# Optimization experiments

Hardware: AMD Instinct MI355X
Metric: run time of the kernel (lower is better)

## Reference

```python
import jax, jax.numpy as jnp
from jax import lax
import numpy as np

N3, N2, N1, N0 = 862, 1723, 3445, 6890  # mesh hierarchy (SMPL 6890 verts)
DEG, K = 16, 4  # nnz/row per Chebyshev support; K = order 3 + 1 supports


def _conv(x, w, b, s):
    y = lax.conv_general_dilated(x, w, (s, s), 'VALID', dimension_numbers=('NCHW', 'OIHW', 'NCHW'))
    return y + b[None, :, None, None]


def _pool(x):
    return lax.reduce_window(x, -jnp.inf, lax.max, (1, 1, 2, 2), (1, 1, 2, 2), 'VALID')


def _lin(x, w, b):
    return x @ w.T + b


def _rodrigues(r):  # [J,3] axis-angle -> [J,3,3] (batch_rodrigues)
    th = jnp.linalg.norm(r, axis=1, keepdims=True) + 1e-8
    k = r / th
    kx, ky, kz = k[:, 0], k[:, 1], k[:, 2]
    z = jnp.zeros_like(kx)
    Km = jnp.stack([z, -kz, ky, kz, z, -kx, -ky, kx, z], axis=1).reshape(-1, 3, 3)
    th = th[:, :, None]
    return jnp.eye(3, dtype=r.dtype)[None] + jnp.sin(th) * Km + (1.0 - jnp.cos(th)) * (Km @ Km)


def _spmm(idx, val, x):  # torch.sparse.mm with fixed nnz/row; idx,val: [N,D]
    return jnp.einsum('nd,ndf->nf', val, x[idx])


def _gcl(x, idx, val, W, b):  # Chebyshev graph conv: sum_k (A_k @ x) @ W_k + b
    return jnp.einsum('knd,kndf,kfo->no', val, x[idx], W) + b


def _basenet(frame, p):
    (c1w, c1b, c2w, c2b, c3w, c3b, c4w, c4b, c5w, c5b, fc1w, fc1b, fc4w, fc4b) = p
    c = _pool(jax.nn.relu(_conv(frame, c1w, c1b, 2)))
    c = _pool(jax.nn.relu(_conv(c, c2w, c2b, 1)))
    c = _pool(jax.nn.relu(_conv(c, c3w, c3b, 1)))
    c = _pool(jax.nn.relu(_conv(c, c4w, c4b, 1)))
    c = _pool(_conv(c, c5w, c5b, 1))  # [1,128,14,14]
    flat = jnp.transpose(c, (0, 3, 2, 1)).reshape(1, -1)  # torch.transpose(c,1,-1).reshape(1,-1)
    return _lin(flat, fc1w, fc1b), jax.nn.relu(_lin(flat, fc4w, fc4b))


def _forward(segmentations, poses, pose_mean, trans,
             c1w, c1b, c2w, c2b, c3w, c3b, c4w, c4b, c5w, c5b,
             fc1w, fc1b, fc2w, fc2b, fc3w, fc3b, fc4w, fc4b,
             fc5w, fc5b, fc6w, fc6b, fc7w, fc7b,
             gW3, gb3, gW2, gb2, gW1, gb1, gW0, gb0,
             av3, av2, av1, av0, uv2, uv1, uv0,
             ai3, ai2, ai1, ai0, ui2, ui1, ui0):
    nf = segmentations.shape[0]
    bp = (c1w, c1b, c2w, c2b, c3w, c3b, c4w, c4b, c5w, c5b, fc1w, fc1b, fc4w, fc4b)
    shape20, pose200 = jax.vmap(lambda f: _basenet(f, bp))(segmentations)  # [F,1,20],[F,1,200]
    pose_feat = jax.nn.relu(_lin(poses, fc5w, fc5b))  # [F,1,200]
    cat = jnp.concatenate([pose200, pose_feat], axis=-1)  # [F,1,400]
    pose_results = _lin(_lin(cat, fc6w, fc6b), fc7w, fc7b)  # [F,1,219]
    pm = pose_mean.at[:3].set(0.0)
    pose_init = _rodrigues(pm.reshape(-1, 3)).reshape(-1)  # [216]
    pct = jnp.concatenate([trans, pose_init])[None, None]  # [1,1,219]
    add = pose_results + pct
    add_poses = add[..., 3:].reshape(nf, -1, 24, 3, 3)
    add_trans = add[..., :3]
    betas_avr = shape20.reshape(-1, 20).mean(0)  # [20]
    betas_val = _lin(betas_avr, fc3w, fc3b)[None]  # [1,10]
    x = _lin(betas_avr, fc2w, fc2b).reshape(N3, 64)
    x = jax.nn.relu(_gcl(x, ai3, av3, gW3, gb3))  # [862,32]
    x = _spmm(ui2, uv2, x)                         # [1723,32]
    x = jax.nn.relu(_gcl(x, ai2, av2, gW2, gb2))  # [1723,16]
    x = _spmm(ui1, uv1, x)                         # [3445,16]
    x = jax.nn.relu(_gcl(x, ai1, av1, gW1, gb1))  # [3445,16]
    x = _spmm(ui0, uv0, x)                         # [6890,16]
    x = jnp.tanh(_gcl(x, ai0, av0, gW0, gb0))     # [6890,3]
    offsets = (x / 10.0)[None]
    return offsets, betas_val, add_poses, add_trans


def setup_inputs():
    ks = iter(jax.random.split(jax.random.key(0), 80))
    f32 = jnp.float32
    nrm = lambda shp, s: jax.random.normal(next(ks), shp, f32) * s
    uni = lambda shp, s: jax.random.uniform(next(ks), shp, f32) * s
    ri = lambda shp, hi: jax.random.randint(next(ks), shp, 0, hi)
    inp = {}
    inp['segmentations'] = nrm((8, 1, 3, 1017, 1017), 1.0)
    inp['poses'] = nrm((8, 1, 75), 1.0)
    inp['pose_mean'] = nrm((72,), 0.3)
    inp['trans'] = jnp.array([0.0, 0.2, -2.3], f32)
    for nm, shp, s in [('c1w', (8, 3, 3, 3), .1), ('c1b', (8,), .01), ('c2w', (16, 8, 3, 3), .1), ('c2b', (16,), .01),
                       ('c3w', (32, 16, 3, 3), .1), ('c3b', (32,), .01), ('c4w', (64, 32, 3, 3), .1), ('c4b', (64,), .01),
                       ('c5w', (128, 64, 3, 3), .1), ('c5b', (128,), .01),
                       ('fc1w', (20, 25088), .01), ('fc1b', (20,), .01), ('fc2w', (55168, 20), .05), ('fc2b', (55168,), .01),
                       ('fc3w', (10, 20), .05), ('fc3b', (10,), .01), ('fc4w', (200, 25088), .01), ('fc4b', (200,), .01),
                       ('fc5w', (200, 75), .05), ('fc5b', (200,), .01), ('fc6w', (100, 400), .05), ('fc6b', (100,), .01),
                       ('fc7w', (219, 100), .05), ('fc7b', (219,), .01),
                       ('gW3', (4, 64, 32), .1), ('gb3', (32,), .01), ('gW2', (4, 32, 16), .1), ('gb2', (16,), .01),
                       ('gW1', (4, 16, 16), .1), ('gb1', (16,), .01), ('gW0', (4, 16, 3), .1), ('gb0', (3,), .01)]:
        inp[nm] = nrm(shp, s)
    for nm, n in [('3', N3), ('2', N2), ('1', N1), ('0', N0)]:
        inp['av' + nm] = uni((K, n, DEG), 0.2)
        inp['ai' + nm] = ri((K, n, DEG), n)
    for nm, n_fine, n_coarse in [('2', N2, N3), ('1', N1, N2), ('0', N0, N1)]:
        inp['uv' + nm] = uni((n_fine, 4), 0.3)
        inp['ui' + nm] = ri((n_fine, 4), n_coarse)
    return inp


def reference(segmentations, poses, pose_mean, trans,
              c1w, c1b, c2w, c2b, c3w, c3b, c4w, c4b, c5w, c5b,
              fc1w, fc1b, fc2w, fc2b, fc3w, fc3b, fc4w, fc4b,
              fc5w, fc5b, fc6w, fc6b, fc7w, fc7b,
              gW3, gb3, gW2, gb2, gW1, gb1, gW0, gb0,
              av3, av2, av1, av0, uv2, uv1, uv0,
              ai3, ai2, ai1, ai0, ui2, ui1, ui0):
    return _forward(segmentations, poses, pose_mean, trans,
                    c1w, c1b, c2w, c2b, c3w, c3b, c4w, c4b, c5w, c5b,
                    fc1w, fc1b, fc2w, fc2b, fc3w, fc3b, fc4w, fc4b,
                    fc5w, fc5b, fc6w, fc6b, fc7w, fc7b,
                    gW3, gb3, gW2, gb2, gW1, gb1, gW0, gb0,
                    av3, av2, av1, av0, uv2, uv1, uv0,
                    ai3, ai2, ai1, ai0, ui2, ui1, ui0)
```

## Files before the change

### kernel.cpp

```cpp
#include <hip/hip_runtime.h>
#include <math.h>

__global__ __launch_bounds__(256) void conv1_lds(
    const float* __restrict__ in, const float* __restrict__ w,
    const float* __restrict__ bias, float* __restrict__ out)
{
    constexpr int Hin = 1017, P = 254;
    __shared__ float li[17][4][65];
    const int f  = blockIdx.y;
    const int ct = blockIdx.x & 3;
    const int rt = blockIdx.x >> 2;
    const int t  = threadIdx.x;
    const int lane = t & 63, wid = t >> 6;
    const int row0 = rt * 16, col0 = ct * 256;
    const float* inf = in + (size_t)f * 3 * Hin * Hin;

    const int ph = rt * 4 + wid, pw = ct * 64 + lane;
    const bool wactive = (ph < P) && (pw < P);

    float acc[32];
    #pragma unroll
    for (int i = 0; i < 32; i++) acc[i] = 0.f;

    for (int ic = 0; ic < 3; ic++) {
        __syncthreads();
        const float* src = inf + (size_t)ic * Hin * Hin;
        #pragma unroll
        for (int i = 0; i < 17; i++) {
            int gr = row0 + i; if (gr > Hin - 1) gr = Hin - 1;
            int gc = col0 + t; if (gc > Hin - 1) gc = Hin - 1;
            li[i][t & 3][t >> 2] = src[(size_t)gr * Hin + gc];
        }
        if (t < 17) {
            int gr = row0 + t; if (gr > Hin - 1) gr = Hin - 1;
            int gc = col0 + 256; if (gc > Hin - 1) gc = Hin - 1;
            li[t][0][64] = src[(size_t)gr * Hin + gc];
        }
        __syncthreads();

        float win[25];
        #pragma unroll
        for (int r = 0; r < 5; r++)
            #pragma unroll
            for (int c = 0; c < 5; c++)
                win[r * 5 + c] = li[4 * wid + r][c & 3][lane + (c >> 2)];

        #pragma unroll
        for (int oc = 0; oc < 8; oc++) {
            float wr[9];
            #pragma unroll
            for (int j = 0; j < 9; j++) wr[j] = w[(oc * 3 + ic) * 9 + j];
            #pragma unroll
            for (int py = 0; py < 2; py++)
                #pragma unroll
                for (int px = 0; px < 2; px++) {
                    float s = acc[(oc * 2 + py) * 2 + px];
                    #pragma unroll
                    for (int kh = 0; kh < 3; kh++)
                        #pragma unroll
                        for (int kw = 0; kw < 3; kw++)
                            s += wr[kh * 3 + kw] * win[(2 * py + kh) * 5 + (2 * px + kw)];
                    acc[(oc * 2 + py) * 2 + px] = s;
                }
        }
    }

    if (wactive) {
        #pragma unroll
        for (int oc = 0; oc < 8; oc++) {
            float m = fmaxf(fmaxf(acc[oc * 4 + 0], acc[oc * 4 + 1]),
                            fmaxf(acc[oc * 4 + 2], acc[oc * 4 + 3]));
            m = fmaxf(m + bias[oc], 0.f);
            out[(((size_t)f * 8 + oc) * P + ph) * P + pw] = m;
        }
    }
}

template<int IC, int OCG, bool RELU, bool FLATOUT>
__global__ __launch_bounds__(256) void conv_pool_s1(
    const float* __restrict__ in, const float* __restrict__ w,
    const float* __restrict__ bias, float* __restrict__ out,
    int Hin, int P, int OC)
{
    const int f = blockIdx.y, g = blockIdx.z;
    int tid = blockIdx.x * 256 + threadIdx.x;
    if (tid >= P * P) return;
    int ph = tid / P, pw = tid % P;
    const float* inf = in + ((size_t)f * IC) * Hin * Hin + (size_t)(2 * ph) * Hin + 2 * pw;
    const float* wg = w + (size_t)g * OCG * IC * 9;

    float acc[OCG * 4];
    #pragma unroll
    for (int i = 0; i < OCG * 4; i++) acc[i] = 0.f;

    for (int ic = 0; ic < IC; ic++) {
        const float* p = inf + (size_t)ic * Hin * Hin;
        float win[4][4];
        #pragma unroll
        for (int r = 0; r < 4; r++) {
            float2 a = *(const float2*)(p + (size_t)r * Hin);
            float2 b = *(const float2*)(p + (size_t)r * Hin + 2);
            win[r][0] = a.x; win[r][1] = a.y; win[r][2] = b.x; win[r][3] = b.y;
        }
        #pragma unroll
        for (int oc = 0; oc < OCG; oc++) {
            float wr[9];
            #pragma unroll
            for (int j = 0; j < 9; j++) wr[j] = wg[(oc * IC + ic) * 9 + j];
            #pragma unroll
            for (int py = 0; py < 2; py++)
                #pragma unroll
                for (int px = 0; px < 2; px++) {
                    float s = acc[(oc * 2 + py) * 2 + px];
                    #pragma unroll
                    for (int kh = 0; kh < 3; kh++)
                        #pragma unroll
                        for (int kw = 0; kw < 3; kw++)
                            s += wr[kh * 3 + kw] * win[py + kh][px + kw];
                    acc[(oc * 2 + py) * 2 + px] = s;
                }
        }
    }

    #pragma unroll
    for (int oc = 0; oc < OCG; oc++) {
        float m = fmaxf(fmaxf(acc[oc * 4 + 0], acc[oc * 4 + 1]),
                        fmaxf(acc[oc * 4 + 2], acc[oc * 4 + 3]));
        m += bias[g * OCG + oc];
        if (RELU) m = fmaxf(m, 0.f);
        int ocg = g * OCG + oc;
        if (FLATOUT) {
            out[(size_t)f * (P * P * OC) + (pw * P + ph) * OC + ocg] = m;
        } else {
            out[(((size_t)f * OC + ocg) * P + ph) * P + pw] = m;
        }
    }
}

__global__ __launch_bounds__(256) void fc_head_plus(
    const float* __restrict__ flat,
    const float* __restrict__ fc1w, const float* __restrict__ fc1b,
    const float* __restrict__ fc4w, const float* __restrict__ fc4b,
    const float* __restrict__ poses,
    const float* __restrict__ fc5w, const float* __restrict__ fc5b,
    float* __restrict__ shape20, float* __restrict__ pose200,
    float* __restrict__ pose_feat)
{
    int o = blockIdx.x;
    if (o < 220) {
        const float* W = (o < 20) ? fc1w + (size_t)o * 25088
                                  : fc4w + (size_t)(o - 20) * 25088;
        const float4* W4  = (const float4*)W;
        const float4* fl4 = (const float4*)flat;
        float acc[8];
        #pragma unroll
        for (int f = 0; f < 8; f++) acc[f] = 0.f;
        for (int i = threadIdx.x; i < 6272; i += 256) {
            float4 wv = W4[i];
            #pragma unroll
            for (int f = 0; f < 8; f++) {
                float4 xv = fl4[f * 6272 + i];
                acc[f] += wv.x * xv.x + wv.y * xv.y + wv.z * xv.z + wv.w * xv.w;
            }
        }
        #pragma unroll
        for (int f = 0; f < 8; f++)
            for (int off = 32; off > 0; off >>= 1)
                acc[f] += __shfl_down(acc[f], off, 64);
        __shared__ float red[4][8];
        int wid = threadIdx.x >> 6, lane = threadIdx.x & 63;
        if (lane == 0) {
            #pragma unroll
            for (int f = 0; f < 8; f++) red[wid][f] = acc[f];
        }
        __syncthreads();
        if (threadIdx.x < 8) {
            int f = threadIdx.x;
            float s = red[0][f] + red[1][f] + red[2][f] + red[3][f];
            if (o < 20) shape20[f * 20 + o] = s + fc1b[o];
            else        pose200[f * 200 + (o - 20)] = fmaxf(s + fc4b[o - 20], 0.f);
        }
    } else {
        int t = (o - 220) * 256 + threadIdx.x;
        if (t >= 8 * 200) return;
        int f = t / 200, oo = t % 200;
        float s = fc5b[oo];
        const float* pr = poses + f * 75;
        const float* wr = fc5w + oo * 75;
        #pragma unroll 5
        for (int j = 0; j < 75; j++) s += pr[j] * wr[j];
        pose_feat[f * 200 + oo] = fmaxf(s, 0.f);
    }
}

__global__ __launch_bounds__(256) void mid_fused(
    const float* __restrict__ shape20,
    const float* __restrict__ fc2w, const float* __restrict__ fc2b,
    const float* __restrict__ fc3w, const float* __restrict__ fc3b,
    float* __restrict__ x0, float* __restrict__ out,
    const float* __restrict__ pose200, const float* __restrict__ pose_feat,
    const float* __restrict__ fc6w, const float* __restrict__ fc6b,
    float* __restrict__ t1)
{
    int b = blockIdx.x, t = threadIdx.x;
    if (b < 216) {
        __shared__ float avr[20];
        if (t < 20) {
            float s = 0.f;
            for (int f = 0; f < 8; f++) s += shape20[f * 20 + t];
            avr[t] = s * 0.125f;
        }
        __syncthreads();
        int r = b * 256 + t;
        if (r < 55168) {
            float s = fc2b[r];
            const float4* w4 = (const float4*)(fc2w + (size_t)r * 20);
            #pragma unroll
            for (int q = 0; q < 5; q++) {
                float4 wv = w4[q];
                s += wv.x * avr[q * 4 + 0] + wv.y * avr[q * 4 + 1]
                   + wv.z * avr[q * 4 + 2] + wv.w * avr[q * 4 + 3];
            }
            x0[r] = s;
        }
        if (b == 0 && t < 10) {
            float s = fc3b[t];
            for (int j = 0; j < 20; j++) s += fc3w[t * 20 + j] * avr[j];
            out[20670 + t] = s;
        }
    } else {
        int wv = (b - 216) * 4 + (t >> 6);
        int lane = t & 63;
        if (wv >= 8 * 100) return;
        int f = wv / 100, o = wv % 100;
        float s = 0.f;
        for (int j = lane; j < 400; j += 64) {
            float xv = (j < 200) ? pose200[f * 200 + j] : pose_feat[f * 200 + (j - 200)];
            s += xv * fc6w[o * 400 + j];
        }
        #pragma unroll
        for (int off = 32; off > 0; off >>= 1) s += __shfl_down(s, off, 64);
        if (lane == 0) t1[f * 100 + o] = s + fc6b[o];
    }
}

__global__ __launch_bounds__(256) void fc7_gcl3(
    const float* __restrict__ x0, const int* __restrict__ ai3,
    const float* __restrict__ av3, const float* __restrict__ gW3,
    const float* __restrict__ gb3, float* __restrict__ y3,
    const float* __restrict__ t1, const float* __restrict__ fc7w,
    const float* __restrict__ fc7b, const float* __restrict__ pose_mean,
    const float* __restrict__ trans, float* __restrict__ out)
{
    constexpr int F = 64, O = 32, N = 862;
    __shared__ float h[256];
    __shared__ float pp[256];
    const int b = blockIdx.x;
    const int wid = threadIdx.x >> 6, lane = threadIdx.x & 63;

    if (b < N) {
        const int n = b;
        {
            const int k = wid;
            const int*   ip = ai3 + ((size_t)k * N + n) * 16;
            const float* vp = av3 + ((size_t)k * N + n) * 16;
            float s = 0.f;
            #pragma unroll
            for (int d = 0; d < 16; d++)
                s += vp[d] * x0[(size_t)ip[d] * F + lane];
            h[k * F + lane] = s;
        }
        __syncthreads();
        const int t = threadIdx.x;
        const int o = t & 31, part = t >> 5;
        {
            float s = 0.f;
            const int base = part * 32;
            #pragma unroll 8
            for (int i = 0; i < 32; i++)
                s += h[base + i] * gW3[(size_t)(base + i) * O + o];
            pp[t] = s;
        }
        __syncthreads();
        if (t < O) {
            float s = gb3[t];
            #pragma unroll
            for (int p = 0; p < 8; p++) s += pp[p * O + t];
            y3[(size_t)n * O + t] = fmaxf(s, 0.f);
        }
    } else {
        int wv = (b - N) * 4 + wid;
        if (wv >= 8 * 219) return;
        int f = wv / 219, c = wv % 219;
        float s = t1[f * 100 + lane] * fc7w[c * 100 + lane];
        int j2 = lane + 64;
        if (j2 < 100) s += t1[f * 100 + j2] * fc7w[c * 100 + j2];
        #pragma unroll
        for (int off = 32; off > 0; off >>= 1) s += __shfl_down(s, off, 64);
        if (lane != 0) return;
        s += fc7b[c];
        float pct;
        if (c < 3) {
            pct = trans[c];
        } else {
            int j = (c - 3) / 9, e = (c - 3) % 9;
            float rx = (j == 0) ? 0.f : pose_mean[3 * j + 0];
            float ry = (j == 0) ? 0.f : pose_mean[3 * j + 1];
            float rz = (j == 0) ? 0.f : pose_mean[3 * j + 2];
            float th = sqrtf(rx * rx + ry * ry + rz * rz) + 1e-8f;
            float kx = rx / th, ky = ry / th, kz = rz / th;
            float sn = sinf(th), c2 = 1.f - cosf(th);
            float R[9];
            R[0] = 1.f - c2 * (ky * ky + kz * kz);
            R[1] = -sn * kz + c2 * (kx * ky);
            R[2] =  sn * ky + c2 * (kx * kz);
            R[3] =  sn * kz + c2 * (kx * ky);
            R[4] = 1.f - c2 * (kx * kx + kz * kz);
            R[5] = -sn * kx + c2 * (ky * kz);
            R[6] = -sn * ky + c2 * (kx * kz);
            R[7] =  sn * kx + c2 * (ky * kz);
            R[8] = 1.f - c2 * (kx * kx + ky * ky);
            pct = R[e];
        }
        s += pct;
        if (c < 3) out[22408 + f * 3 + c] = s;
        else       out[20680 + f * 216 + (c - 3)] = s;
    }
}

template<int F, int O, int ACT>
__global__ __launch_bounds__(256) void gcl(
    const float* __restrict__ x, const int* __restrict__ ai,
    const float* __restrict__ av, const float* __restrict__ gW,
    const float* __restrict__ gb, float* __restrict__ y, int N)
{
    constexpr int VPB = 64 / F;
    constexpr int OUTS = VPB * O;
    constexpr int PARTS = (256 / OUTS) >= 16 ? 16 :
                          ((256 / OUTS) >= 8 ? 8 :
                          ((256 / OUTS) >= 4 ? 4 : 2));
    constexpr int CH = 4 * F / PARTS;
    constexpr int HS = 4 * F + 4;
    __shared__ float h[VPB][HS];
    __shared__ float pp[OUTS * PARTS];

    const int k = threadIdx.x >> 6;
    const int lane = threadIdx.x & 63;
    const int vl = (VPB == 1) ? 0 : lane / F;
    const int fl = lane % F;
    const int n = blockIdx.x * VPB + vl;
    if (n < N) {
        const int*   ip = ai + ((size_t)k * N + n) * 16;
        const float* vp = av + ((size_t)k * N + n) * 16;
        float s = 0.f;
        #pragma unroll
        for (int d = 0; d < 16; d++)
            s += vp[d] * x[(size_t)ip[d] * F + fl];
        h[vl][k * F + fl] = s;
    }
    __syncthreads();

    const int t = threadIdx.x;
    if (t < OUTS * PARTS) {
        const int idx = t % OUTS;
        const int part = t / OUTS;
        const int v = idx / O, o = idx % O;
        float s = 0.f;
        const int base = part * CH;
        #pragma unroll
        for (int i = 0; i < CH; i++)
            s += h[v][base + i] * gW[(size_t)(base + i) * O + o];
        pp[part * OUTS + idx] = s;
    }
    __syncthreads();
    if (t < OUTS) {
        const int v = t / O, o = t % O;
        const int n2 = blockIdx.x * VPB + v;
        if (n2 < N) {
            float s = gb[o];
            #pragma unroll
            for (int p = 0; p < PARTS; p++) s += pp[p * OUTS + t];
            if (ACT == 0) s = fmaxf(s, 0.f);
            else          s = tanhf(s) * 0.1f;
            y[(size_t)n2 * O + o] = s;
        }
    }
}

template<int F>
__global__ __launch_bounds__(256) void spmm(
    const float* __restrict__ x, const int* __restrict__ ui,
    const float* __restrict__ uv, float* __restrict__ y, int N)
{
    int t = blockIdx.x * 256 + threadIdx.x;
    if (t >= N * F) return;
    int n = t / F, f = t % F;
    float s = 0.f;
    #pragma unroll
    for (int j = 0; j < 4; j++)
        s += uv[n * 4 + j] * x[(size_t)ui[n * 4 + j] * F + f];
    y[t] = s;
}

extern "C" void kernel_launch(void* const* d_in, const int* in_sizes, int n_in,
                              void* d_out, int out_size, void* d_ws, size_t ws_size,
                              hipStream_t stream) {
    (void)in_sizes; (void)n_in; (void)out_size; (void)ws_size;

    const float* seg   = (const float*)d_in[0];
    const float* poses = (const float*)d_in[1];
    const float* pmean = (const float*)d_in[2];
    const float* trans = (const float*)d_in[3];
    const float* c1w = (const float*)d_in[4];  const float* c1b = (const float*)d_in[5];
    const float* c2w = (const float*)d_in[6];  const float* c2b = (const float*)d_in[7];
    const float* c3w = (const float*)d_in[8];  const float* c3b = (const float*)d_in[9];
    const float* c4w = (const float*)d_in[10]; const float* c4b = (const float*)d_in[11];
    const float* c5w = (const float*)d_in[12]; const float* c5b = (const float*)d_in[13];
    const float* fc1w = (const float*)d_in[14]; const float* fc1b = (const float*)d_in[15];
    const float* fc2w = (const float*)d_in[16]; const float* fc2b = (const float*)d_in[17];
    const float* fc3w = (const float*)d_in[18]; const float* fc3b = (const float*)d_in[19];
    const float* fc4w = (const float*)d_in[20]; const float* fc4b = (const float*)d_in[21];
    const float* fc5w = (const float*)d_in[22]; const float* fc5b = (const float*)d_in[23];
    const float* fc6w = (const float*)d_in[24]; const float* fc6b = (const float*)d_in[25];
    const float* fc7w = (const float*)d_in[26]; const float* fc7b = (const float*)d_in[27];
    const float* gW3 = (const float*)d_in[28]; const float* gb3 = (const float*)d_in[29];
    const float* gW2 = (const float*)d_in[30]; const float* gb2 = (const float*)d_in[31];
    const float* gW1 = (const float*)d_in[32]; const float* gb1 = (const float*)d_in[33];
    const float* gW0 = (const float*)d_in[34]; const float* gb0 = (const float*)d_in[35];
    const float* av3 = (const float*)d_in[36]; const int* ai3 = (const int*)d_in[37];
    const float* av2 = (const float*)d_in[38]; const int* ai2 = (const int*)d_in[39];
    const float* av1 = (const float*)d_in[40]; const int* ai1 = (const int*)d_in[41];
    const float* av0 = (const float*)d_in[42]; const int* ai0 = (const int*)d_in[43];
    const float* uv2 = (const float*)d_in[44]; const int* ui2 = (const int*)d_in[45];
    const float* uv1 = (const float*)d_in[46]; const int* ui1 = (const int*)d_in[47];
    const float* uv0 = (const float*)d_in[48]; const int* ui0 = (const int*)d_in[49];

    float* W = (float*)d_ws;
    float* out = (float*)d_out;

    float* pool1 = W + 0;
    float* pool2 = W + 4129024;
    float* pool3 = W + 0;
    float* pool4 = W + 4129024;
    float* flat5 = W + 4589824;
    float* shape20 = W + 1000000;
    float* pose200 = shape20 + 160;
    float* x0  = pose200 + 1600;
    float* y3  = x0 + 55168;
    float* x2  = y3 + 27584;
    float* y2  = x2 + 55136;
    float* x1  = y2 + 27568;
    float* y1  = x1 + 55120;
    float* x0u = y1 + 55120;
    float* pose_feat = x0u + 110240;
    float* t1 = pose_feat + 1600;

    conv1_lds<<<dim3(256, 8), 256, 0, stream>>>(seg, c1w, c1b, pool1);
    conv_pool_s1<8, 8, true, false>
        <<<dim3(63, 8, 2), 256, 0, stream>>>(pool1, c2w, c2b, pool2, 254, 126, 16);
    conv_pool_s1<16, 4, true, false>
        <<<dim3(16, 8, 8), 256, 0, stream>>>(pool2, c3w, c3b, pool3, 126, 62, 32);
    conv_pool_s1<32, 2, true, false>
        <<<dim3(4, 8, 32), 256, 0, stream>>>(pool3, c4w, c4b, pool4, 62, 30, 64);
    conv_pool_s1<64, 2, false, true>
        <<<dim3(1, 8, 64), 256, 0, stream>>>(pool4, c5w, c5b, flat5, 30, 14, 128);

    fc_head_plus<<<dim3(227), 256, 0, stream>>>(flat5, fc1w, fc1b, fc4w, fc4b,
                                                poses, fc5w, fc5b,
                                                shape20, pose200, pose_feat);
    mid_fused<<<dim3(416), 256, 0, stream>>>(shape20, fc2w, fc2b, fc3w, fc3b, x0, out,
                                             pose200, pose_feat, fc6w, fc6b, t1);

    fc7_gcl3<<<dim3(1300), 256, 0, stream>>>(x0, ai3, av3, gW3, gb3, y3,
                                             t1, fc7w, fc7b, pmean, trans, out);
    spmm<32>      <<<dim3(216),  256, 0, stream>>>(y3,  ui2, uv2, x2, 1723);
    gcl<32, 16, 0><<<dim3(862),  256, 0, stream>>>(x2,  ai2, av2, gW2, gb2, y2, 1723);
    spmm<16>      <<<dim3(216),  256, 0, stream>>>(y2,  ui1, uv1, x1, 3445);
    gcl<16, 16, 0><<<dim3(862),  256, 0, stream>>>(x1,  ai1, av1, gW1, gb1, y1, 3445);
    spmm<16>      <<<dim3(431),  256, 0, stream>>>(y1,  ui0, uv0, x0u, 6890);
    gcl<16, 3, 1> <<<dim3(1723), 256, 0, stream>>>(x0u, ai0, av0, gW0, gb0, out, 6890);
}
```

Before: 169.9 us.

## Fold upsampling SpMM into Chebyshev adjacency by precomputing composed sparse operator

Each graph-conv level's adjacency (16 nnz/row) is composed with the preceding upsampling matrix (4 nnz/row) into a 64-nnz/row operator. The operator is built inside the existing mid_fused kernel through extra blocks. This removes three spmm launches and their intermediate buffers. The price is four times as many gathers per GCL row, plus rebuilding the large composed index/value arrays on every call, which adds memory traffic.

```diff
diff --git a/kernel.cpp b/kernel.cpp
--- a/kernel.cpp
+++ b/kernel.cpp
@@ -193,14 +193,38 @@
     }
 }
 
-__global__ __launch_bounds__(256) void mid_fused(
+__device__ __forceinline__ void build_C_range(
+    int tid, int Nf, const int* __restrict__ ai, const float* __restrict__ av,
+    const int* __restrict__ ui, const float* __restrict__ uv,
+    int* __restrict__ ci, float* __restrict__ cv)
+{
+    if (tid >= 4 * Nf * 16) return;
+    int m = ai[tid];
+    float a = av[tid];
+    #pragma unroll
+    for (int j = 0; j < 4; j++) {
+        ci[(size_t)tid * 4 + j] = ui[(size_t)m * 4 + j];
+        cv[(size_t)tid * 4 + j] = a * uv[(size_t)m * 4 + j];
+    }
+}
+
+__global__ __launch_bounds__(256) void mid_fused_plus(
     const float* __restrict__ shape20,
     const float* __restrict__ fc2w, const float* __restrict__ fc2b,
     const float* __restrict__ fc3w, const float* __restrict__ fc3b,
     float* __restrict__ x0, float* __restrict__ out,
     const float* __restrict__ pose200, const float* __restrict__ pose_feat,
     const float* __restrict__ fc6w, const float* __restrict__ fc6b,
-    float* __restrict__ t1)
+    float* __restrict__ t1,
+    const int* __restrict__ ai2, const float* __restrict__ av2,
+    const int* __restrict__ ui2, const float* __restrict__ uv2,
+    const int* __restrict__ ai1, const float* __restrict__ av1,
+    const int* __restrict__ ui1, const float* __restrict__ uv1,
+    const int* __restrict__ ai0, const float* __restrict__ av0,
+    const int* __restrict__ ui0, const float* __restrict__ uv0,
+    int* __restrict__ ci2, float* __restrict__ cv2,
+    int* __restrict__ ci1, float* __restrict__ cv1,
+    int* __restrict__ ci0, float* __restrict__ cv0)
 {
     int b = blockIdx.x, t = threadIdx.x;
     if (b < 216) {
@@ -228,7 +252,7 @@
             for (int j = 0; j < 20; j++) s += fc3w[t * 20 + j] * avr[j];
             out[20670 + t] = s;
         }
-    } else {
+    } else if (b < 416) {
         int wv = (b - 216) * 4 + (t >> 6);
         int lane = t & 63;
         if (wv >= 8 * 100) return;
@@ -241,6 +265,14 @@
         #pragma unroll
         for (int off = 32; off > 0; off >>= 1) s += __shfl_down(s, off, 64);
         if (lane == 0) t1[f * 100 + o] = s + fc6b[o];
+    } else {
+        int bc = b - 416;
+        if (bc < 431)
+            build_C_range(bc * 256 + t, 1723, ai2, av2, ui2, uv2, ci2, cv2);
+        else if (bc < 431 + 862)
+            build_C_range((bc - 431) * 256 + t, 3445, ai1, av1, ui1, uv1, ci1, cv1);
+        else
+            build_C_range((bc - 1293) * 256 + t, 6890, ai0, av0, ui0, uv0, ci0, cv0);
     }
 }
 
@@ -329,9 +361,9 @@
 }
 
 template<int F, int O, int ACT>
-__global__ __launch_bounds__(256) void gcl(
-    const float* __restrict__ x, const int* __restrict__ ai,
-    const float* __restrict__ av, const float* __restrict__ gW,
+__global__ __launch_bounds__(256) void gclC(
+    const float* __restrict__ y_prev, const int* __restrict__ ci,
+    const float* __restrict__ cv, const float* __restrict__ gW,
     const float* __restrict__ gb, float* __restrict__ y, int N)
 {
     constexpr int VPB = 64 / F;
@@ -350,12 +382,12 @@
     const int fl = lane % F;
     const int n = blockIdx.x * VPB + vl;
     if (n < N) {
-        const int*   ip = ai + ((size_t)k * N + n) * 16;
-        const float* vp = av + ((size_t)k * N + n) * 16;
+        const int*   ip = ci + ((size_t)k * N + n) * 64;
+        const float* vp = cv + ((size_t)k * N + n) * 64;
         float s = 0.f;
-        #pragma unroll
-        for (int d = 0; d < 16; d++)
-            s += vp[d] * x[(size_t)ip[d] * F + fl];
+        #pragma unroll 4
+        for (int e = 0; e < 64; e++)
+            s += vp[e] * y_prev[(size_t)ip[e] * F + fl];
         h[vl][k * F + fl] = s;
     }
     __syncthreads();
@@ -385,21 +417,6 @@
             y[(size_t)n2 * O + o] = s;
         }
     }
-}
-
-template<int F>
-__global__ __launch_bounds__(256) void spmm(
-    const float* __restrict__ x, const int* __restrict__ ui,
-    const float* __restrict__ uv, float* __restrict__ y, int N)
-{
-    int t = blockIdx.x * 256 + threadIdx.x;
-    if (t >= N * F) return;
-    int n = t / F, f = t % F;
-    float s = 0.f;
-    #pragma unroll
-    for (int j = 0; j < 4; j++)
-        s += uv[n * 4 + j] * x[(size_t)ui[n * 4 + j] * F + f];
-    y[t] = s;
 }
 
 extern "C" void kernel_launch(void* const* d_in, const int* in_sizes, int n_in,
@@ -447,13 +464,17 @@
     float* pose200 = shape20 + 160;
     float* x0  = pose200 + 1600;
     float* y3  = x0 + 55168;
-    float* x2  = y3 + 27584;
-    float* y2  = x2 + 55136;
-    float* x1  = y2 + 27568;
-    float* y1  = x1 + 55120;
-    float* x0u = y1 + 55120;
-    float* pose_feat = x0u + 110240;
+    float* y2  = y3 + 27584;
+    float* y1  = y2 + 27568;
+    float* pose_feat = y1 + 55120;
     float* t1 = pose_feat + 1600;
+
+    int*   ci2 = (int*)  (W + 8000000);
+    float* cv2 =          W + 8500000;
+    int*   ci1 = (int*)  (W + 9000000);
+    float* cv1 =          W + 10000000;
+    int*   ci0 = (int*)  (W + 11000000);
+    float* cv0 =          W + 13000000;
 
     conv1_lds<<<dim3(256, 8), 256, 0, stream>>>(seg, c1w, c1b, pool1);
     conv_pool_s1<8, 8, true, false>
@@ -468,15 +489,15 @@
     fc_head_plus<<<dim3(227), 256, 0, stream>>>(flat5, fc1w, fc1b, fc4w, fc4b,
                                                 poses, fc5w, fc5b,
                                                 shape20, pose200, pose_feat);
-    mid_fused<<<dim3(416), 256, 0, stream>>>(shape20, fc2w, fc2b, fc3w, fc3b, x0, out,
-                                             pose200, pose_feat, fc6w, fc6b, t1);
+    mid_fused_plus<<<dim3(3432), 256, 0, stream>>>(
+        shape20, fc2w, fc2b, fc3w, fc3b, x0, out,
+        pose200, pose_feat, fc6w, fc6b, t1,
+        ai2, av2, ui2, uv2, ai1, av1, ui1, uv1, ai0, av0, ui0, uv0,
+        ci2, cv2, ci1, cv1, ci0, cv0);
 
     fc7_gcl3<<<dim3(1300), 256, 0, stream>>>(x0, ai3, av3, gW3, gb3, y3,
                                              t1, fc7w, fc7b, pmean, trans, out);
-    spmm<32>      <<<dim3(216),  256, 0, stream>>>(y3,  ui2, uv2, x2, 1723);
-    gcl<32, 16, 0><<<dim3(862),  256, 0, stream>>>(x2,  ai2, av2, gW2, gb2, y2, 1723);
-    spmm<16>      <<<dim3(216),  256, 0, stream>>>(y2,  ui1, uv1, x1, 3445);
-    gcl<16, 16, 0><<<dim3(862),  256, 0, stream>>>(x1,  ai1, av1, gW1, gb1, y1, 3445);
-    spmm<16>      <<<dim3(431),  256, 0, stream>>>(y1,  ui0, uv0, x0u, 6890);
-    gcl<16, 3, 1> <<<dim3(1723), 256, 0, stream>>>(x0u, ai0, av0, gW0, gb0, out, 6890);
-}
+    gclC<32, 16, 0><<<dim3(862),  256, 0, stream>>>(y3, ci2, cv2, gW2, gb2, y2, 1723);
+    gclC<16, 16, 0><<<dim3(862),  256, 0, stream>>>(y2, ci1, cv1, gW1, gb1, y1, 3445);
+    gclC<16, 3, 1> <<<dim3(1723), 256, 0, stream>>>(y1, ci0, cv0, gW0, gb0, out, 6890);
+}
```

New measurement: 186.9 us. 10.0% more time.
